# Performance work log

Hardware: AMD Instinct MI355X
Metric: run time of the kernel (lower is better)

Reference implementation:

```python
import jax, jax.numpy as jnp
import numpy as np

B, S, D, H = 4, 1024, 1024, 16
HD = D // H  # head_dim = 64


def setup_inputs() -> dict:
    key = jax.random.key(0)
    ks = jax.random.split(key, 16)
    w = lambda k: jax.random.normal(k, (D, D), dtype=jnp.float32) * 0.02
    b = lambda k: jax.random.normal(k, (D,), dtype=jnp.float32) * 0.02
    x = jax.random.normal(ks[0], (B, S, D), dtype=jnp.float32)
    mask = jnp.tril(jnp.ones((S, S), dtype=jnp.int32))[None, None]  # causal [1,1,S,S]
    bar_indices = jax.random.randint(ks[1], (S,), 0, S, dtype=jnp.int64)
    beat_indices = jax.random.randint(ks[2], (S,), 0, S, dtype=jnp.int64)
    return {
        "x": x, "mask": mask, "bar_indices": bar_indices, "beat_indices": beat_indices,
        "Wq": w(ks[3]), "bq": b(ks[4]), "Wk": w(ks[5]), "bk": b(ks[6]),
        "Wv": w(ks[7]), "bv": b(ks[8]),
        "W_bark": w(ks[9]), "b_bark": b(ks[10]),
        "W_beatk": w(ks[11]), "b_beatk": b(ks[12]),
        "Wo": w(ks[13]), "bo": b(ks[14]),
    }


def reference(x, mask, bar_indices, beat_indices, Wq, bq, Wk, bk, Wv, bv,
              W_bark, b_bark, W_beatk, b_beatk, Wo, bo):
    Bs, Sl, Dm = x.shape
    heads, hd = H, Dm // H

    def proj(t, W, b):  # torch Linear: t @ W.T + b, then split heads -> [B,H,S,hd]
        y = t @ W.T + b
        return y.reshape(Bs, -1, heads, hd).transpose(0, 2, 1, 3)

    q = proj(x, Wq, bq)
    k = proj(x, Wk, bk)
    v = proj(x, Wv, bv)
    scale = 1.0 / jnp.sqrt(jnp.asarray(hd, x.dtype))

    scores = jnp.einsum('bhqd,bhkd->bhqk', q, k) * scale

    # hierarchical bar bias (bar_query is computed but unused in the original)
    bar_k = proj(x[:, bar_indices], W_bark, b_bark)
    scores = scores + 0.2 * (jnp.einsum('bhqd,bhkd->bhqk', q, bar_k) * scale)

    # hierarchical beat bias
    beat_k = proj(x[:, beat_indices], W_beatk, b_beatk)
    scores = scores + 0.1 * (jnp.einsum('bhqd,bhkd->bhqk', q, beat_k) * scale)

    scores = jnp.where(mask == 0, jnp.asarray(-1e9, scores.dtype), scores)
    attn = jax.nn.softmax(scores, axis=-1)  # dropout is identity in eval

    out = jnp.einsum('bhqk,bhkd->bhqd', attn, v)
    out = out.transpose(0, 2, 1, 3).reshape(Bs, Sl, Dm)
    return out @ Wo.T + bo
```

## Files before the change

### kernel.cpp

```cpp
#include <hip/hip_runtime.h>
#include <hip/hip_bf16.h>


typedef __bf16 bf16x8 __attribute__((ext_vector_type(8)));
typedef __bf16 bf16x4 __attribute__((ext_vector_type(4)));
typedef float  f32x4  __attribute__((ext_vector_type(4)));

#define DMODEL 1024

#define ASYNC_LOAD16(gp, lp)                                                  \
    __builtin_amdgcn_global_load_lds(                                         \
        (const __attribute__((address_space(1))) unsigned int*)(gp),          \
        (__attribute__((address_space(3))) unsigned int*)(lp), 16, 0, 0)

__global__ __launch_bounds__(256) void cvt_kernel(
    const float* __restrict__ x,
    const float* __restrict__ Wq, const float* __restrict__ Wk,
    const float* __restrict__ Wv, const float* __restrict__ Wbar,
    const float* __restrict__ Wbeat, const float* __restrict__ Wo,
    __bf16* __restrict__ dst)
{
    const int g = blockIdx.x * 256 + threadIdx.x;
    const size_t e = (size_t)g * 8;
    const int seg = (int)(e >> 20);
    const float* src; size_t off; float s = 1.0f;
    if (seg < 4)       { src = x;     off = e; }
    else if (seg == 4) { src = Wq;    off = e - ((size_t)4 << 20); }
    else if (seg == 5) { src = Wk;    off = e - ((size_t)5 << 20); }
    else if (seg == 6) { src = Wv;    off = e - ((size_t)6 << 20); }
    else if (seg == 7) { src = Wbar;  off = e - ((size_t)7 << 20); s = 0.2f; }
    else if (seg == 8) { src = Wbeat; off = e - ((size_t)8 << 20); s = 0.1f; }
    else               { src = Wo;    off = e - ((size_t)9 << 20); }
    const float4 a = *(const float4*)&src[off];
    const float4 b = *(const float4*)&src[off + 4];
    bf16x8 v;
    v[0] = (__bf16)(a.x * s); v[1] = (__bf16)(a.y * s);
    v[2] = (__bf16)(a.z * s); v[3] = (__bf16)(a.w * s);
    v[4] = (__bf16)(b.x * s); v[5] = (__bf16)(b.y * s);
    v[6] = (__bf16)(b.z * s); v[7] = (__bf16)(b.w * s);
    *(bf16x8*)&dst[e] = v;
}

__global__ __launch_bounds__(256) void proj_kernel(
    const __bf16* __restrict__ xb, const __bf16* __restrict__ attnbuf,
    const __bf16* __restrict__ Wqb, const __bf16* __restrict__ Wkb,
    const __bf16* __restrict__ Wvb, const __bf16* __restrict__ Wbarb,
    const __bf16* __restrict__ Wbeatb, const __bf16* __restrict__ Wob,
    const float* __restrict__ bq, const float* __restrict__ bk,
    const float* __restrict__ bv, const float* __restrict__ bbar,
    const float* __restrict__ bbeat, const float* __restrict__ bo,
    const int* __restrict__ bar_idx, const int* __restrict__ beat_idx,
    __bf16* __restrict__ qbuf, __bf16* __restrict__ keffbuf,
    __bf16* __restrict__ vtbuf, float* __restrict__ outbuf,
    int mode_base)
{
    const int mode = mode_base + blockIdx.y;
    const int tile = blockIdx.x;
    const int m0 = (tile >> 3) << 7;
    const int n0 = (tile & 7) << 7;

    __shared__ __align__(16) __bf16 Alds[128 * 32];
    __shared__ __align__(16) __bf16 Blds[128 * 32];

    const int t    = threadIdx.x;
    const int w    = t >> 6;
    const int lane = t & 63;
    const int l15  = lane & 15;
    const int quad = lane >> 4;
    const int wm   = (w >> 1) << 6;
    const int wn   = (w & 1) << 6;
    const int srow = t >> 2;
    const int scol = (t & 3) * 8;

    const __bf16* Aptr = (mode == 3) ? attnbuf : xb;
    const int nterms = (mode == 1) ? 3 : 1;

    f32x4 acc[4][4];
    for (int i = 0; i < 4; ++i)
        for (int j = 0; j < 4; ++j)
            acc[i][j] = {0.f, 0.f, 0.f, 0.f};

    for (int term = 0; term < nterms; ++term) {
        const __bf16* Wterm =
            (mode == 0) ? Wqb :
            (mode == 2) ? Wvb :
            (mode == 3) ? Wob :
            (term == 0) ? Wkb : (term == 1) ? Wbarb : Wbeatb;

        int arow0, arow1;
        if (mode != 1 || term == 0) {
            arow0 = m0 + srow;
            arow1 = m0 + 64 + srow;
        } else {
            const int* gi = (term == 1) ? bar_idx : beat_idx;
            const int bbase = m0 & ~1023;
            arow0 = bbase + gi[(m0 & 1023) + srow];
            arow1 = bbase + gi[(m0 & 1023) + 64 + srow];
        }
        const __bf16* gA0 = Aptr + (size_t)arow0 * DMODEL + scol;
        const __bf16* gA1 = Aptr + (size_t)arow1 * DMODEL + scol;
        const __bf16* gB0 = Wterm + (size_t)(n0 + srow) * DMODEL + scol;
        const __bf16* gB1 = Wterm + (size_t)(n0 + 64 + srow) * DMODEL + scol;
        __bf16* lA0 = &Alds[w * 512];
        __bf16* lA1 = &Alds[2048 + w * 512];
        __bf16* lB0 = &Blds[w * 512];
        __bf16* lB1 = &Blds[2048 + w * 512];

        for (int kk = 0; kk < 32; ++kk) {
            const int k0 = kk * 32;
            ASYNC_LOAD16(gA0 + k0, lA0);
            ASYNC_LOAD16(gA1 + k0, lA1);
            ASYNC_LOAD16(gB0 + k0, lB0);
            ASYNC_LOAD16(gB1 + k0, lB1);
            __syncthreads();

            bf16x8 af[4], bfr[4];
            for (int i = 0; i < 4; ++i)
                af[i] = *(const bf16x8*)&Alds[(wm + i * 16 + l15) * 32 + quad * 8];
            for (int j = 0; j < 4; ++j)
                bfr[j] = *(const bf16x8*)&Blds[(wn + j * 16 + l15) * 32 + quad * 8];

            for (int i = 0; i < 4; ++i)
                for (int j = 0; j < 4; ++j)
                    acc[i][j] = __builtin_amdgcn_mfma_f32_16x16x32_bf16(
                        af[i], bfr[j], acc[i][j], 0, 0, 0);
            __syncthreads();
        }
    }

    for (int j = 0; j < 4; ++j) {
        const int col = n0 + wn + j * 16 + l15;
        float bias;
        if (mode == 0)      bias = bq[col];
        else if (mode == 1) bias = bk[col] + 0.2f * bbar[col] + 0.1f * bbeat[col];
        else if (mode == 2) bias = bv[col];
        else                bias = bo[col];

        for (int i = 0; i < 4; ++i) {
            const int rowbase = m0 + wm + i * 16 + quad * 4;
            if (mode == 2) {
                const int bb = rowbase >> 10;
                const int sb = rowbase & 1023;
                bf16x4 vv;
                for (int r = 0; r < 4; ++r) vv[r] = (__bf16)(acc[i][j][r] + bias);
                *(bf16x4*)&vtbuf[((size_t)(bb * 1024 + col)) * 1024 + sb] = vv;
            } else if (mode == 3) {
                for (int r = 0; r < 4; ++r)
                    outbuf[(size_t)(rowbase + r) * DMODEL + col] =
                        acc[i][j][r] + bias;
            } else if (mode == 0) {
                for (int r = 0; r < 4; ++r)
                    qbuf[(size_t)(rowbase + r) * DMODEL + col] =
                        (__bf16)((acc[i][j][r] + bias) * 0.125f);
            } else {
                for (int r = 0; r < 4; ++r)
                    keffbuf[(size_t)(rowbase + r) * DMODEL + col] =
                        (__bf16)(acc[i][j][r] + bias);
            }
        }
    }
}

__global__ __launch_bounds__(256) void oproj_kernel(
    const __bf16* __restrict__ attnb, const __bf16* __restrict__ Wob,
    const float* __restrict__ bo, float* __restrict__ outb)
{
    const int tile = blockIdx.x;
    const int m0 = (tile >> 3) << 6;
    const int n0 = (tile & 7) << 7;

    __shared__ __align__(16) __bf16 Alds[64 * 32];
    __shared__ __align__(16) __bf16 Blds[128 * 32];

    const int t    = threadIdx.x;
    const int w    = t >> 6;
    const int lane = t & 63;
    const int l15  = lane & 15;
    const int quad = lane >> 4;
    const int wm   = (w >> 1) << 5;
    const int wn   = (w & 1) << 6;
    const int srow = t >> 2;
    const int scol = (t & 3) * 8;

    const __bf16* gA  = attnb + (size_t)(m0 + srow) * DMODEL + scol;
    const __bf16* gB0 = Wob + (size_t)(n0 + srow) * DMODEL + scol;
    const __bf16* gB1 = Wob + (size_t)(n0 + 64 + srow) * DMODEL + scol;
    __bf16* lA  = &Alds[w * 512];
    __bf16* lB0 = &Blds[w * 512];
    __bf16* lB1 = &Blds[2048 + w * 512];

    f32x4 acc[2][4];
    for (int i = 0; i < 2; ++i)
        for (int j = 0; j < 4; ++j)
            acc[i][j] = {0.f, 0.f, 0.f, 0.f};

    for (int kk = 0; kk < 32; ++kk) {
        const int k0 = kk * 32;
        ASYNC_LOAD16(gA + k0, lA);
        ASYNC_LOAD16(gB0 + k0, lB0);
        ASYNC_LOAD16(gB1 + k0, lB1);
        __syncthreads();

        bf16x8 af[2], bfr[4];
        for (int i = 0; i < 2; ++i)
            af[i] = *(const bf16x8*)&Alds[(wm + i * 16 + l15) * 32 + quad * 8];
        for (int j = 0; j < 4; ++j)
            bfr[j] = *(const bf16x8*)&Blds[(wn + j * 16 + l15) * 32 + quad * 8];

        for (int i = 0; i < 2; ++i)
            for (int j = 0; j < 4; ++j)
                acc[i][j] = __builtin_amdgcn_mfma_f32_16x16x32_bf16(
                    af[i], bfr[j], acc[i][j], 0, 0, 0);
        __syncthreads();
    }

    for (int j = 0; j < 4; ++j) {
        const int col = n0 + wn + j * 16 + l15;
        const float bias = bo[col];
        for (int i = 0; i < 2; ++i) {
            const int rowbase = m0 + wm + i * 16 + quad * 4;
            for (int r = 0; r < 4; ++r)
                outb[(size_t)(rowbase + r) * DMODEL + col] = acc[i][j][r] + bias;
        }
    }
}

__global__ __launch_bounds__(256) void attn_kernel(
    const __bf16* __restrict__ qbuf, const __bf16* __restrict__ keffbuf,
    const __bf16* __restrict__ vtbuf, __bf16* __restrict__ attnbuf)
{
    const int bh = blockIdx.y;
    const int b  = bh >> 4;
    const int h  = bh & 15;
    const int qt = blockIdx.x;
    const int q0 = qt * 64;

    __shared__ __align__(16) __bf16 Klds[64][72];
    __shared__ __align__(16) __bf16 Vlds[64][72];
    __shared__ __align__(16) __bf16 Plds[4][16][72];

    const int t    = threadIdx.x;
    const int w    = t >> 6;
    const int lane = t & 63;
    const int l15  = lane & 15;
    const int quad = lane >> 4;

    const __bf16* qbase =
        qbuf + (size_t)(b * 1024 + q0 + w * 16 + l15) * DMODEL + h * 64;
    bf16x8 qf0 = *(const bf16x8*)&qbase[quad * 8];
    bf16x8 qf1 = *(const bf16x8*)&qbase[32 + quad * 8];

    bf16x8 ones;
    for (int i = 0; i < 8; ++i) ones[i] = (__bf16)1.0f;

    f32x4 o[4];
    for (int i = 0; i < 4; ++i) o[i] = {0.f, 0.f, 0.f, 0.f};
    f32x4 lacc = {0.f, 0.f, 0.f, 0.f};

    const int srow = t >> 2;
    const int scol = (t & 3) * 16;

    const __bf16* kbase = keffbuf + (size_t)(b * 1024) * DMODEL + h * 64;
    const __bf16* vtb   = vtbuf + (size_t)(b * 1024 + h * 64) * 1024;

    for (int j = 0; j <= qt; ++j) {
        const __bf16* kg = kbase + (size_t)(j * 64 + srow) * DMODEL + scol;
        *(bf16x8*)&Klds[srow][scol]     = *(const bf16x8*)kg;
        *(bf16x8*)&Klds[srow][scol + 8] = *(const bf16x8*)(kg + 8);
        const __bf16* vg = vtb + (size_t)srow * 1024 + j * 64 + scol;
        *(bf16x8*)&Vlds[srow][scol]     = *(const bf16x8*)vg;
        *(bf16x8*)&Vlds[srow][scol + 8] = *(const bf16x8*)(vg + 8);
        __syncthreads();

        f32x4 sc[4];
        for (int nt = 0; nt < 4; ++nt) {
            sc[nt] = {0.f, 0.f, 0.f, 0.f};
            bf16x8 kf0 = *(const bf16x8*)&Klds[nt * 16 + l15][quad * 8];
            bf16x8 kf1 = *(const bf16x8*)&Klds[nt * 16 + l15][32 + quad * 8];
            sc[nt] = __builtin_amdgcn_mfma_f32_16x16x32_bf16(qf0, kf0, sc[nt], 0, 0, 0);
            sc[nt] = __builtin_amdgcn_mfma_f32_16x16x32_bf16(qf1, kf1, sc[nt], 0, 0, 0);
        }

        if (j == qt) {
            const int qrow_base = q0 + w * 16 + quad * 4;
            for (int nt = 0; nt < 4; ++nt) {
                const int kcol = j * 64 + nt * 16 + l15;
                for (int r = 0; r < 4; ++r)
                    if (kcol > qrow_base + r) sc[nt][r] = -1e30f;
            }
        }

        for (int nt = 0; nt < 4; ++nt)
            for (int r = 0; r < 4; ++r)
                sc[nt][r] = __expf(sc[nt][r]);

        for (int nt = 0; nt < 4; ++nt)
            for (int r = 0; r < 4; ++r)
                Plds[w][quad * 4 + r][nt * 16 + l15] = (__bf16)sc[nt][r];
        asm volatile("s_waitcnt lgkmcnt(0)" ::: "memory");

        bf16x8 pf0 = *(const bf16x8*)&Plds[w][l15][quad * 8];
        bf16x8 pf1 = *(const bf16x8*)&Plds[w][l15][32 + quad * 8];

        lacc = __builtin_amdgcn_mfma_f32_16x16x32_bf16(pf0, ones, lacc, 0, 0, 0);
        lacc = __builtin_amdgcn_mfma_f32_16x16x32_bf16(pf1, ones, lacc, 0, 0, 0);

        for (int nd = 0; nd < 4; ++nd) {
            bf16x8 vf0 = *(const bf16x8*)&Vlds[nd * 16 + l15][quad * 8];
            bf16x8 vf1 = *(const bf16x8*)&Vlds[nd * 16 + l15][32 + quad * 8];
            o[nd] = __builtin_amdgcn_mfma_f32_16x16x32_bf16(pf0, vf0, o[nd], 0, 0, 0);
            o[nd] = __builtin_amdgcn_mfma_f32_16x16x32_bf16(pf1, vf1, o[nd], 0, 0, 0);
        }
        __syncthreads();
    }

    float rinv[4];
    for (int r = 0; r < 4; ++r) rinv[r] = 1.0f / lacc[r];
    for (int nd = 0; nd < 4; ++nd) {
        for (int r = 0; r < 4; ++r) {
            const int row = q0 + w * 16 + quad * 4 + r;
            attnbuf[(size_t)(b * 1024 + row) * DMODEL + h * 64 + nd * 16 + l15] =
                (__bf16)(o[nd][r] * rinv[r]);
        }
    }
}

extern "C" void kernel_launch(void* const* d_in, const int* in_sizes, int n_in,
                              void* d_out, int out_size, void* d_ws, size_t ws_size,
                              hipStream_t stream) {
    const float* x     = (const float*)d_in[0];
    const int* bar     = (const int*)d_in[2];
    const int* beat    = (const int*)d_in[3];
    const float* Wq    = (const float*)d_in[4];
    const float* bq    = (const float*)d_in[5];
    const float* Wk    = (const float*)d_in[6];
    const float* bk    = (const float*)d_in[7];
    const float* Wv    = (const float*)d_in[8];
    const float* bv    = (const float*)d_in[9];
    const float* Wbar  = (const float*)d_in[10];
    const float* bbar  = (const float*)d_in[11];
    const float* Wbeat = (const float*)d_in[12];
    const float* bbeat = (const float*)d_in[13];
    const float* Wo    = (const float*)d_in[14];
    const float* bo    = (const float*)d_in[15];

    const size_t M1 = (size_t)1 << 20;
    __bf16* xb     = (__bf16*)d_ws;
    __bf16* Wqb    = xb + 4 * M1;
    __bf16* Wkb    = Wqb + M1;
    __bf16* Wvb    = Wkb + M1;
    __bf16* Wbarb  = Wvb + M1;
    __bf16* Wbeatb = Wbarb + M1;
    __bf16* Wob    = Wbeatb + M1;
    __bf16* qbuf   = Wob + M1;
    __bf16* keff   = qbuf + 4 * M1;
    __bf16* vt     = keff + 4 * M1;
    __bf16* attn   = vt + 4 * M1;
    float*  outb   = (float*)d_out;

    cvt_kernel<<<5120, 256, 0, stream>>>(x, Wq, Wk, Wv, Wbar, Wbeat, Wo, xb);

    proj_kernel<<<dim3(256, 3), 256, 0, stream>>>(
        xb, attn, Wqb, Wkb, Wvb, Wbarb, Wbeatb, Wob,
        bq, bk, bv, bbar, bbeat, bo, bar, beat,
        qbuf, keff, vt, outb, 0);

    attn_kernel<<<dim3(16, 64), 256, 0, stream>>>(qbuf, keff, vt, attn);

    oproj_kernel<<<512, 256, 0, stream>>>(attn, Wob, bo, outb);
}
```

Baseline: 236.6 us.

## Drop attention LDS staging, shrink out-proj tiles, reorder grids and projection modes

The attention kernel stops staging K and V tiles in shared memory. Each wave now loads its MFMA fragments straight from global memory, which removes two block barriers per key tile but makes every wave re-fetch the same K/V data. The attention grid swaps its axes so consecutive blocks span batch-heads rather than query tiles. The output projection tile shrinks from 64x128 to 64x64, doubling the block count for better CU occupancy. The projection kernel drops its unused mode-3 path and remaps blockIdx.y so the three-term K projection blocks are scheduled first.

Result: slower. 267.9 us (+13.2%).

```diff
diff --git a/kernel.cpp b/kernel.cpp
--- a/kernel.cpp
+++ b/kernel.cpp
@@ -42,19 +42,19 @@
 }
 
 __global__ __launch_bounds__(256) void proj_kernel(
-    const __bf16* __restrict__ xb, const __bf16* __restrict__ attnbuf,
+    const __bf16* __restrict__ xb,
     const __bf16* __restrict__ Wqb, const __bf16* __restrict__ Wkb,
     const __bf16* __restrict__ Wvb, const __bf16* __restrict__ Wbarb,
-    const __bf16* __restrict__ Wbeatb, const __bf16* __restrict__ Wob,
+    const __bf16* __restrict__ Wbeatb,
     const float* __restrict__ bq, const float* __restrict__ bk,
     const float* __restrict__ bv, const float* __restrict__ bbar,
-    const float* __restrict__ bbeat, const float* __restrict__ bo,
+    const float* __restrict__ bbeat,
     const int* __restrict__ bar_idx, const int* __restrict__ beat_idx,
     __bf16* __restrict__ qbuf, __bf16* __restrict__ keffbuf,
-    __bf16* __restrict__ vtbuf, float* __restrict__ outbuf,
-    int mode_base)
+    __bf16* __restrict__ vtbuf)
 {
-    const int mode = mode_base + blockIdx.y;
+    const int lut[3] = {1, 0, 2};
+    const int mode = lut[blockIdx.y];
     const int tile = blockIdx.x;
     const int m0 = (tile >> 3) << 7;
     const int n0 = (tile & 7) << 7;
@@ -72,7 +72,6 @@
     const int srow = t >> 2;
     const int scol = (t & 3) * 8;
 
-    const __bf16* Aptr = (mode == 3) ? attnbuf : xb;
     const int nterms = (mode == 1) ? 3 : 1;
 
     f32x4 acc[4][4];
@@ -84,7 +83,6 @@
         const __bf16* Wterm =
             (mode == 0) ? Wqb :
             (mode == 2) ? Wvb :
-            (mode == 3) ? Wob :
             (term == 0) ? Wkb : (term == 1) ? Wbarb : Wbeatb;
 
         int arow0, arow1;
@@ -97,8 +95,8 @@
             arow0 = bbase + gi[(m0 & 1023) + srow];
             arow1 = bbase + gi[(m0 & 1023) + 64 + srow];
         }
-        const __bf16* gA0 = Aptr + (size_t)arow0 * DMODEL + scol;
-        const __bf16* gA1 = Aptr + (size_t)arow1 * DMODEL + scol;
+        const __bf16* gA0 = xb + (size_t)arow0 * DMODEL + scol;
+        const __bf16* gA1 = xb + (size_t)arow1 * DMODEL + scol;
         const __bf16* gB0 = Wterm + (size_t)(n0 + srow) * DMODEL + scol;
         const __bf16* gB1 = Wterm + (size_t)(n0 + 64 + srow) * DMODEL + scol;
         __bf16* lA0 = &Alds[w * 512];
@@ -133,8 +131,7 @@
         float bias;
         if (mode == 0)      bias = bq[col];
         else if (mode == 1) bias = bk[col] + 0.2f * bbar[col] + 0.1f * bbeat[col];
-        else if (mode == 2) bias = bv[col];
-        else                bias = bo[col];
+        else                bias = bv[col];
 
         for (int i = 0; i < 4; ++i) {
             const int rowbase = m0 + wm + i * 16 + quad * 4;
@@ -144,10 +141,6 @@
                 bf16x4 vv;
                 for (int r = 0; r < 4; ++r) vv[r] = (__bf16)(acc[i][j][r] + bias);
                 *(bf16x4*)&vtbuf[((size_t)(bb * 1024 + col)) * 1024 + sb] = vv;
-            } else if (mode == 3) {
-                for (int r = 0; r < 4; ++r)
-                    outbuf[(size_t)(rowbase + r) * DMODEL + col] =
-                        acc[i][j][r] + bias;
             } else if (mode == 0) {
                 for (int r = 0; r < 4; ++r)
                     qbuf[(size_t)(rowbase + r) * DMODEL + col] =
@@ -166,11 +159,11 @@
     const float* __restrict__ bo, float* __restrict__ outb)
 {
     const int tile = blockIdx.x;
-    const int m0 = (tile >> 3) << 6;
-    const int n0 = (tile & 7) << 7;
+    const int m0 = (tile >> 4) << 6;
+    const int n0 = (tile & 15) << 6;
 
     __shared__ __align__(16) __bf16 Alds[64 * 32];
-    __shared__ __align__(16) __bf16 Blds[128 * 32];
+    __shared__ __align__(16) __bf16 Blds[64 * 32];
 
     const int t    = threadIdx.x;
     const int w    = t >> 6;
@@ -178,43 +171,40 @@
     const int l15  = lane & 15;
     const int quad = lane >> 4;
     const int wm   = (w >> 1) << 5;
-    const int wn   = (w & 1) << 6;
+    const int wn   = (w & 1) << 5;
     const int srow = t >> 2;
     const int scol = (t & 3) * 8;
 
-    const __bf16* gA  = attnb + (size_t)(m0 + srow) * DMODEL + scol;
-    const __bf16* gB0 = Wob + (size_t)(n0 + srow) * DMODEL + scol;
-    const __bf16* gB1 = Wob + (size_t)(n0 + 64 + srow) * DMODEL + scol;
-    __bf16* lA  = &Alds[w * 512];
-    __bf16* lB0 = &Blds[w * 512];
-    __bf16* lB1 = &Blds[2048 + w * 512];
-
-    f32x4 acc[2][4];
+    const __bf16* gA = attnb + (size_t)(m0 + srow) * DMODEL + scol;
+    const __bf16* gB = Wob + (size_t)(n0 + srow) * DMODEL + scol;
+    __bf16* lA = &Alds[w * 512];
+    __bf16* lB = &Blds[w * 512];
+
+    f32x4 acc[2][2];
     for (int i = 0; i < 2; ++i)
-        for (int j = 0; j < 4; ++j)
+        for (int j = 0; j < 2; ++j)
             acc[i][j] = {0.f, 0.f, 0.f, 0.f};
 
     for (int kk = 0; kk < 32; ++kk) {
         const int k0 = kk * 32;
         ASYNC_LOAD16(gA + k0, lA);
-        ASYNC_LOAD16(gB0 + k0, lB0);
-        ASYNC_LOAD16(gB1 + k0, lB1);
+        ASYNC_LOAD16(gB + k0, lB);
         __syncthreads();
 
-        bf16x8 af[2], bfr[4];
+        bf16x8 af[2], bfr[2];
         for (int i = 0; i < 2; ++i)
             af[i] = *(const bf16x8*)&Alds[(wm + i * 16 + l15) * 32 + quad * 8];
-        for (int j = 0; j < 4; ++j)
+        for (int j = 0; j < 2; ++j)
             bfr[j] = *(const bf16x8*)&Blds[(wn + j * 16 + l15) * 32 + quad * 8];
 
         for (int i = 0; i < 2; ++i)
-            for (int j = 0; j < 4; ++j)
+            for (int j = 0; j < 2; ++j)
                 acc[i][j] = __builtin_amdgcn_mfma_f32_16x16x32_bf16(
                     af[i], bfr[j], acc[i][j], 0, 0, 0);
         __syncthreads();
     }
 
-    for (int j = 0; j < 4; ++j) {
+    for (int j = 0; j < 2; ++j) {
         const int col = n0 + wn + j * 16 + l15;
         const float bias = bo[col];
         for (int i = 0; i < 2; ++i) {
@@ -229,14 +219,12 @@
     const __bf16* __restrict__ qbuf, const __bf16* __restrict__ keffbuf,
     const __bf16* __restrict__ vtbuf, __bf16* __restrict__ attnbuf)
 {
-    const int bh = blockIdx.y;
+    const int bh = blockIdx.x;
     const int b  = bh >> 4;
     const int h  = bh & 15;
-    const int qt = blockIdx.x;
+    const int qt = blockIdx.y;
     const int q0 = qt * 64;
 
-    __shared__ __align__(16) __bf16 Klds[64][72];
-    __shared__ __align__(16) __bf16 Vlds[64][72];
     __shared__ __align__(16) __bf16 Plds[4][16][72];
 
     const int t    = threadIdx.x;
@@ -257,26 +245,16 @@
     for (int i = 0; i < 4; ++i) o[i] = {0.f, 0.f, 0.f, 0.f};
     f32x4 lacc = {0.f, 0.f, 0.f, 0.f};
 
-    const int srow = t >> 2;
-    const int scol = (t & 3) * 16;
-
-    const __bf16* kbase = keffbuf + (size_t)(b * 1024) * DMODEL + h * 64;
-    const __bf16* vtb   = vtbuf + (size_t)(b * 1024 + h * 64) * 1024;
+    const __bf16* kb = keffbuf + (size_t)(b * 1024) * DMODEL + h * 64;
+    const __bf16* vb = vtbuf + (size_t)(b * 1024 + h * 64) * 1024;
 
     for (int j = 0; j <= qt; ++j) {
-        const __bf16* kg = kbase + (size_t)(j * 64 + srow) * DMODEL + scol;
-        *(bf16x8*)&Klds[srow][scol]     = *(const bf16x8*)kg;
-        *(bf16x8*)&Klds[srow][scol + 8] = *(const bf16x8*)(kg + 8);
-        const __bf16* vg = vtb + (size_t)srow * 1024 + j * 64 + scol;
-        *(bf16x8*)&Vlds[srow][scol]     = *(const bf16x8*)vg;
-        *(bf16x8*)&Vlds[srow][scol + 8] = *(const bf16x8*)(vg + 8);
-        __syncthreads();
-
         f32x4 sc[4];
         for (int nt = 0; nt < 4; ++nt) {
+            const __bf16* kr = kb + (size_t)(j * 64 + nt * 16 + l15) * DMODEL;
+            bf16x8 kf0 = *(const bf16x8*)&kr[quad * 8];
+            bf16x8 kf1 = *(const bf16x8*)&kr[32 + quad * 8];
             sc[nt] = {0.f, 0.f, 0.f, 0.f};
-            bf16x8 kf0 = *(const bf16x8*)&Klds[nt * 16 + l15][quad * 8];
-            bf16x8 kf1 = *(const bf16x8*)&Klds[nt * 16 + l15][32 + quad * 8];
             sc[nt] = __builtin_amdgcn_mfma_f32_16x16x32_bf16(qf0, kf0, sc[nt], 0, 0, 0);
             sc[nt] = __builtin_amdgcn_mfma_f32_16x16x32_bf16(qf1, kf1, sc[nt], 0, 0, 0);
         }
@@ -306,12 +284,12 @@
         lacc = __builtin_amdgcn_mfma_f32_16x16x32_bf16(pf1, ones, lacc, 0, 0, 0);
 
         for (int nd = 0; nd < 4; ++nd) {
-            bf16x8 vf0 = *(const bf16x8*)&Vlds[nd * 16 + l15][quad * 8];
-            bf16x8 vf1 = *(const bf16x8*)&Vlds[nd * 16 + l15][32 + quad * 8];
+            const __bf16* vr = vb + (size_t)(nd * 16 + l15) * 1024 + j * 64;
+            bf16x8 vf0 = *(const bf16x8*)&vr[quad * 8];
+            bf16x8 vf1 = *(const bf16x8*)&vr[32 + quad * 8];
             o[nd] = __builtin_amdgcn_mfma_f32_16x16x32_bf16(pf0, vf0, o[nd], 0, 0, 0);
             o[nd] = __builtin_amdgcn_mfma_f32_16x16x32_bf16(pf1, vf1, o[nd], 0, 0, 0);
         }
-        __syncthreads();
     }
 
     float rinv[4];
@@ -361,11 +339,11 @@
     cvt_kernel<<<5120, 256, 0, stream>>>(x, Wq, Wk, Wv, Wbar, Wbeat, Wo, xb);
 
     proj_kernel<<<dim3(256, 3), 256, 0, stream>>>(
-        xb, attn, Wqb, Wkb, Wvb, Wbarb, Wbeatb, Wob,
-        bq, bk, bv, bbar, bbeat, bo, bar, beat,
-        qbuf, keff, vt, outb, 0);
-
-    attn_kernel<<<dim3(16, 64), 256, 0, stream>>>(qbuf, keff, vt, attn);
-
-    oproj_kernel<<<512, 256, 0, stream>>>(attn, Wob, bo, outb);
-}
+        xb, Wqb, Wkb, Wvb, Wbarb, Wbeatb,
+        bq, bk, bv, bbar, bbeat, bar, beat,
+        qbuf, keff, vt);
+
+    attn_kernel<<<dim3(64, 16), 256, 0, stream>>>(qbuf, keff, vt, attn);
+
+    oproj_kernel<<<1024, 256, 0, stream>>>(attn, Wob, bo, outb);
+}
```
